# Kernel tuning notes

Hardware: AMD Instinct MI355X
Metric: run time of the kernel (lower is better)

Reference implementation:

```python
import jax, jax.numpy as jnp
import numpy as np

N_NODES = 100000
N_EDGES = 600000
F_IN = 128
F_OUT = 128


def setup_inputs() -> dict:
    key = jax.random.key(0)
    ks = jax.random.split(key, 9)
    stdv = 1.0 / np.sqrt(F_OUT)
    return {
        "x": jax.random.normal(ks[0], (N_NODES, F_IN), dtype=jnp.float32),
        "weight": jax.random.uniform(ks[1], (F_IN, F_OUT), dtype=jnp.float32, minval=-stdv, maxval=stdv),
        "bias": jax.random.uniform(ks[2], (F_OUT,), dtype=jnp.float32, minval=-stdv, maxval=stdv),
        "vals0": jax.random.uniform(ks[3], (N_EDGES,), dtype=jnp.float32),
        "vals1": jax.random.uniform(ks[4], (N_EDGES,), dtype=jnp.float32),
        "rows0": jax.random.randint(ks[5], (N_EDGES,), 0, N_NODES, dtype=jnp.int32),
        "cols0": jax.random.randint(ks[6], (N_EDGES,), 0, N_NODES, dtype=jnp.int32),
        "rows1": jax.random.randint(ks[7], (N_EDGES,), 0, N_NODES, dtype=jnp.int32),
        "cols1": jax.random.randint(ks[8], (N_EDGES,), 0, N_NODES, dtype=jnp.int32),
    }


def _spmm(rows, cols, vals, dense, n):
    # COO sparse [n,n] @ dense [n,f]: gather source rows, scale, scatter-add to dest rows
    msgs = dense[cols] * vals[:, None]          # [E, f]
    return jax.ops.segment_sum(msgs, rows, num_segments=n)


def reference(x, weight, bias, vals0, vals1, rows0, cols0, rows1, cols1):
    n = x.shape[0]
    support = x @ weight                         # [N, F_OUT] dense GEMM
    out = _spmm(rows0, cols0, vals0, support, n) \
        + _spmm(rows1, cols1, vals1, support, n)
    return out + bias
```

## Files before the change

kernel.cpp:

```cpp
#include <hip/hip_runtime.h>


#define FDIM 128
#define EPB 2048

typedef __attribute__((ext_vector_type(8))) short short8;
typedef __attribute__((ext_vector_type(4))) float floatx4;

__device__ __forceinline__ unsigned short f32_to_bf16(float f) {
    unsigned int u = __float_as_uint(f);
    unsigned int r = u + 0x7fffu + ((u >> 16) & 1u);
    return (unsigned short)(r >> 16);
}

__device__ __forceinline__ float bf16_lo(unsigned int u) {
    return __uint_as_float((u & 0xffffu) << 16);
}
__device__ __forceinline__ float bf16_hi(unsigned int u) {
    return __uint_as_float(u & 0xffff0000u);
}

__global__ __launch_bounds__(256) void prep(const float* __restrict__ w,
                                            unsigned short* __restrict__ wt,
                                            int* __restrict__ zero_ptr, int zero_ints) {
    int bid = blockIdx.x;
    if (bid < 64) {
        int idx = bid * 256 + threadIdx.x;
        int nn = idx >> 7, k = idx & 127;
        wt[idx] = f32_to_bf16(w[(size_t)k * FDIM + nn]);
    } else {
        int idx = (bid - 64) * 256 + threadIdx.x;
        if (idx < zero_ints) zero_ptr[idx] = 0;
    }
}

__global__ __launch_bounds__(256) void gemm_hist(const float* __restrict__ x,
                                                 const unsigned short* __restrict__ wt,
                                                 unsigned short* __restrict__ support,
                                                 int n,
                                                 const int* __restrict__ rows0,
                                                 const int* __restrict__ rows1,
                                                 int* __restrict__ count,
                                                 int* __restrict__ rank,
                                                 int E, int GB) {
    if ((int)blockIdx.x >= GB) {
        int gid = (blockIdx.x - GB) * 256 + threadIdx.x;
        if (gid < 2 * E) {
            int r = (gid < E) ? rows0[gid] : rows1[gid - E];
            rank[gid] = atomicAdd(&count[r], 1);
        }
        return;
    }
    const int tid = threadIdx.x;
    const int wv = tid >> 6, lane = tid & 63;
    const int quad = lane >> 4, lr = lane & 15;
    const int rbase = blockIdx.x * 256 + wv * 64;
    if (rbase >= n) return;

    short8 b[8][4];
    #pragma unroll
    for (int nt = 0; nt < 8; ++nt)
        #pragma unroll
        for (int ks = 0; ks < 4; ++ks)
            b[nt][ks] = *(const short8*)(wt + (size_t)(nt * 16 + lr) * FDIM + ks * 32 + quad * 8);

    for (int t = 0; t < 4; ++t) {
        const int row0 = rbase + t * 16;
        if (row0 >= n) break;
        const int arow = row0 + lr;
        const bool rowok = arow < n;
        const float* xr = x + (size_t)arow * FDIM;

        floatx4 acc[8];
        #pragma unroll
        for (int nt = 0; nt < 8; ++nt) acc[nt] = (floatx4)0.f;

        #pragma unroll
        for (int ks = 0; ks < 4; ++ks) {
            float4 lo = rowok ? *(const float4*)(xr + ks * 32 + quad * 8)     : make_float4(0.f,0.f,0.f,0.f);
            float4 hi = rowok ? *(const float4*)(xr + ks * 32 + quad * 8 + 4) : make_float4(0.f,0.f,0.f,0.f);
            short8 a;
            a[0] = (short)f32_to_bf16(lo.x); a[1] = (short)f32_to_bf16(lo.y);
            a[2] = (short)f32_to_bf16(lo.z); a[3] = (short)f32_to_bf16(lo.w);
            a[4] = (short)f32_to_bf16(hi.x); a[5] = (short)f32_to_bf16(hi.y);
            a[6] = (short)f32_to_bf16(hi.z); a[7] = (short)f32_to_bf16(hi.w);
            #pragma unroll
            for (int nt = 0; nt < 8; ++nt)
                acc[nt] = __builtin_amdgcn_mfma_f32_16x16x32_bf16(a, b[nt][ks], acc[nt], 0, 0, 0);
        }

        #pragma unroll
        for (int i = 0; i < 4; ++i) {
            int row = row0 + quad * 4 + i;
            if (row < n) {
                #pragma unroll
                for (int nt = 0; nt < 8; ++nt)
                    support[(size_t)row * FDIM + nt * 16 + lr] = f32_to_bf16(acc[nt][i]);
            }
        }
    }
}

__device__ __forceinline__ int block_incl_scan(int v, int tid, int* lds) {
    int lane = tid & 63, wv = tid >> 6;
    #pragma unroll
    for (int d = 1; d < 64; d <<= 1) {
        int y = __shfl_up(v, d);
        if (lane >= d) v += y;
    }
    if (lane == 63) lds[wv] = v;
    __syncthreads();
    if (wv == 0 && lane < 4) {
        int s = lds[lane];
        #pragma unroll
        for (int d = 1; d < 4; d <<= 1) {
            int y = __shfl_up(s, d);
            if (lane >= d) s += y;
        }
        lds[4 + lane] = s;
    }
    __syncthreads();
    int add = (wv > 0) ? lds[4 + wv - 1] : 0;
    return v + add;
}

__global__ __launch_bounds__(256) void rowptr_scan(const int* __restrict__ count,
                                                   int* __restrict__ rowptr,
                                                   int* __restrict__ gcur, int n) {
    __shared__ int lds[8];
    __shared__ int base;
    int tid = threadIdx.x;
    int idx = blockIdx.x * 256 + tid;
    int v = (idx < n) ? count[idx] : 0;
    int inc = block_incl_scan(v, tid, lds);
    if (tid == 255) base = atomicAdd(gcur, inc);
    __syncthreads();
    if (idx < n) rowptr[idx] = base + inc - v;
}

__global__ __launch_bounds__(256) void scatter_row(
    const int* __restrict__ rows0, const int* __restrict__ cols0, const float* __restrict__ vals0,
    const int* __restrict__ rows1, const int* __restrict__ cols1, const float* __restrict__ vals1,
    const int* __restrict__ rank, const int* __restrict__ rowptr,
    int2* __restrict__ rec, int E, int nper) {
    const int p = blockIdx.x & 7;
    const int base = (blockIdx.x >> 3) * EPB;
    const int tid = threadIdx.x;
    #pragma unroll
    for (int it = 0; it < EPB / 256; ++it) {
        int gid = base + it * 256 + tid;
        if (gid < 2 * E) {
            int r = (gid < E) ? rows0[gid] : rows1[gid - E];
            if (r / nper == p) {
                int c; float v;
                if (gid < E) { c = cols0[gid]; v = vals0[gid]; }
                else         { int e = gid - E; c = cols1[e]; v = vals1[e]; }
                rec[rowptr[r] + rank[gid]] = make_int2(c, __float_as_int(v));
            }
        }
    }
}

__global__ __launch_bounds__(256) void pull_csr(const unsigned short* __restrict__ support,
                                                const int* __restrict__ rowptr,
                                                const int* __restrict__ count,
                                                const int2* __restrict__ rec,
                                                const float* __restrict__ bias,
                                                float* __restrict__ out, int n) {
    int wid = (blockIdx.x * 256 + threadIdx.x) >> 6;
    int lane = threadIdx.x & 63;
    if (wid >= n) return;
    int beg = rowptr[wid];
    int end = beg + count[wid];
    float ax = 0.f, ay = 0.f;
    const char* sp = (const char*)support;
    const unsigned loff = (unsigned)lane << 2;

    for (int base = beg; base < end; base += 64) {
        int m = end - base; if (m > 64) m = 64;
        long long pk = 0;
        if (lane < m) pk = *(const long long*)&rec[base + lane];
        int j = 0;
        for (; j + 8 <= m; j += 8) {
            long long p0 = __shfl(pk, j);
            long long p1 = __shfl(pk, j + 1);
            long long p2 = __shfl(pk, j + 2);
            long long p3 = __shfl(pk, j + 3);
            long long p4 = __shfl(pk, j + 4);
            long long p5 = __shfl(pk, j + 5);
            long long p6 = __shfl(pk, j + 6);
            long long p7 = __shfl(pk, j + 7);
            unsigned u0 = *(const unsigned*)(sp + (((unsigned)p0) << 8) + loff);
            unsigned u1 = *(const unsigned*)(sp + (((unsigned)p1) << 8) + loff);
            unsigned u2 = *(const unsigned*)(sp + (((unsigned)p2) << 8) + loff);
            unsigned u3 = *(const unsigned*)(sp + (((unsigned)p3) << 8) + loff);
            unsigned u4 = *(const unsigned*)(sp + (((unsigned)p4) << 8) + loff);
            unsigned u5 = *(const unsigned*)(sp + (((unsigned)p5) << 8) + loff);
            unsigned u6 = *(const unsigned*)(sp + (((unsigned)p6) << 8) + loff);
            unsigned u7 = *(const unsigned*)(sp + (((unsigned)p7) << 8) + loff);
            float v0 = __int_as_float((int)(p0 >> 32));
            float v1 = __int_as_float((int)(p1 >> 32));
            float v2 = __int_as_float((int)(p2 >> 32));
            float v3 = __int_as_float((int)(p3 >> 32));
            float v4 = __int_as_float((int)(p4 >> 32));
            float v5 = __int_as_float((int)(p5 >> 32));
            float v6 = __int_as_float((int)(p6 >> 32));
            float v7 = __int_as_float((int)(p7 >> 32));
            ax += v0 * bf16_lo(u0); ay += v0 * bf16_hi(u0);
            ax += v1 * bf16_lo(u1); ay += v1 * bf16_hi(u1);
            ax += v2 * bf16_lo(u2); ay += v2 * bf16_hi(u2);
            ax += v3 * bf16_lo(u3); ay += v3 * bf16_hi(u3);
            ax += v4 * bf16_lo(u4); ay += v4 * bf16_hi(u4);
            ax += v5 * bf16_lo(u5); ay += v5 * bf16_hi(u5);
            ax += v6 * bf16_lo(u6); ay += v6 * bf16_hi(u6);
            ax += v7 * bf16_lo(u7); ay += v7 * bf16_hi(u7);
        }
        for (; j + 4 <= m; j += 4) {
            long long p0 = __shfl(pk, j);
            long long p1 = __shfl(pk, j + 1);
            long long p2 = __shfl(pk, j + 2);
            long long p3 = __shfl(pk, j + 3);
            unsigned u0 = *(const unsigned*)(sp + (((unsigned)p0) << 8) + loff);
            unsigned u1 = *(const unsigned*)(sp + (((unsigned)p1) << 8) + loff);
            unsigned u2 = *(const unsigned*)(sp + (((unsigned)p2) << 8) + loff);
            unsigned u3 = *(const unsigned*)(sp + (((unsigned)p3) << 8) + loff);
            float v0 = __int_as_float((int)(p0 >> 32));
            float v1 = __int_as_float((int)(p1 >> 32));
            float v2 = __int_as_float((int)(p2 >> 32));
            float v3 = __int_as_float((int)(p3 >> 32));
            ax += v0 * bf16_lo(u0); ay += v0 * bf16_hi(u0);
            ax += v1 * bf16_lo(u1); ay += v1 * bf16_hi(u1);
            ax += v2 * bf16_lo(u2); ay += v2 * bf16_hi(u2);
            ax += v3 * bf16_lo(u3); ay += v3 * bf16_hi(u3);
        }
        for (; j < m; ++j) {
            long long p = __shfl(pk, j);
            unsigned u = *(const unsigned*)(sp + (((unsigned)p) << 8) + loff);
            float v = __int_as_float((int)(p >> 32));
            ax += v * bf16_lo(u); ay += v * bf16_hi(u);
        }
    }
    float2 b = *(const float2*)(bias + lane * 2);
    *(float2*)(out + (size_t)wid * FDIM + lane * 2) = make_float2(ax + b.x, ay + b.y);
}

__global__ __launch_bounds__(256) void init_bias(const float* __restrict__ bias,
                                                 float* __restrict__ out, int n) {
    int idx = blockIdx.x * 256 + threadIdx.x;
    int total = n * (FDIM / 4);
    if (idx < total) {
        int j = (idx & (FDIM / 4 - 1)) * 4;
        float4 b = *(const float4*)(bias + j);
        *(float4*)(out + (size_t)idx * 4) = b;
    }
}

__global__ __launch_bounds__(256) void scatter_bf16(
    const unsigned short* __restrict__ support,
    const int* __restrict__ rows0, const int* __restrict__ cols0, const float* __restrict__ vals0,
    const int* __restrict__ rows1, const int* __restrict__ cols1, const float* __restrict__ vals1,
    float* __restrict__ out, int E) {
    int gid = blockIdx.x * 256 + threadIdx.x;
    int lane = gid & 63;
    int eg = gid >> 6;
    if (eg >= 2 * E) return;
    int r, c; float v;
    if (eg < E) { r = rows0[eg]; c = cols0[eg]; v = vals0[eg]; }
    else        { int e = eg - E; r = rows1[e]; c = cols1[e]; v = vals1[e]; }
    unsigned int u = *(const unsigned int*)(support + (size_t)c * FDIM + lane * 2);
    float sx = bf16_lo(u);
    float sy = bf16_hi(u);
    float* op = out + (size_t)r * FDIM + lane * 2;
    atomicAdd(op,     sx * v);
    atomicAdd(op + 1, sy * v);
}

static inline size_t align256(size_t v) { return (v + 255) & ~(size_t)255; }

extern "C" void kernel_launch(void* const* d_in, const int* in_sizes, int n_in,
                              void* d_out, int out_size, void* d_ws, size_t ws_size,
                              hipStream_t stream) {
    const float* x     = (const float*)d_in[0];
    const float* w     = (const float*)d_in[1];
    const float* bias  = (const float*)d_in[2];
    const float* vals0 = (const float*)d_in[3];
    const float* vals1 = (const float*)d_in[4];
    const int*   rows0 = (const int*)d_in[5];
    const int*   cols0 = (const int*)d_in[6];
    const int*   rows1 = (const int*)d_in[7];
    const int*   cols1 = (const int*)d_in[8];
    const int n = in_sizes[0] / FDIM;
    const int E = in_sizes[3];
    float* out = (float*)d_out;

    const int NB = (n + 255) / 256;

    size_t off = 0;
    unsigned short* support = (unsigned short*)((char*)d_ws + off);
    off = align256(off + (size_t)n * FDIM * 2);
    unsigned short* wt = (unsigned short*)((char*)d_ws + off);
    off = align256(off + (size_t)FDIM * FDIM * 2);
    size_t count_off = off;
    int*  count  = (int*)((char*)d_ws + off);  off = align256(off + (size_t)n * 4);
    int*  gcur   = (int*)((char*)d_ws + off);  off = align256(off + 4);
    size_t zero_bytes = off - count_off;
    int*  rowptr = (int*)((char*)d_ws + off);  off = align256(off + (size_t)n * 4);
    int*  rank   = (int*)((char*)d_ws + off);  off = align256(off + (size_t)2 * E * 4);
    int2* rec    = (int2*)((char*)d_ws + off); off = align256(off + (size_t)2 * E * 8);

    const bool fits = off <= ws_size;
    const int GB = (n + 255) / 256;
    const int HB = fits ? (2 * E + 255) / 256 : 0;

    int zero_ints = fits ? (int)(zero_bytes / 4) : 0;
    int zb = (zero_ints + 255) / 256;
    prep<<<64 + zb, 256, 0, stream>>>(w, wt, (int*)((char*)d_ws + count_off), zero_ints);

    gemm_hist<<<GB + HB, 256, 0, stream>>>(x, wt, support, n,
                                           rows0, rows1, count, rank, E, GB);

    if (fits) {
        rowptr_scan<<<NB, 256, 0, stream>>>(count, rowptr, gcur, n);
        int nper = (n + 7) / 8;
        int ntiles = (2 * E + EPB - 1) / EPB;
        scatter_row<<<ntiles * 8, 256, 0, stream>>>(rows0, cols0, vals0,
                                                    rows1, cols1, vals1,
                                                    rank, rowptr, rec, E, nper);
        pull_csr<<<(n + 3) / 4, 256, 0, stream>>>(support, rowptr, count, rec, bias, out, n);
    } else {
        int total4 = n * (FDIM / 4);
        init_bias<<<(total4 + 255) / 256, 256, 0, stream>>>(bias, out, n);
        long long tthreads = 2LL * E * 64;
        int blocks = (int)((tthreads + 255) / 256);
        scatter_bf16<<<blocks, 256, 0, stream>>>(support, rows0, cols0, vals0,
                                                 rows1, cols1, vals1, out, E);
    }
}
```

Measured before the change: 264.4 us.

## Split GEMM from histogram, stage weights in LDS, use atomic cursors for CSR scatter

The fused GEMM+histogram kernel is split in two. The GEMM now stages the bf16 weight tile in LDS and processes 64 rows per block, where before each wave held the weights in registers across 64 rows. The histogram no longer stores per-edge ranks. Instead, scatter claims slots with atomics on a per-row cursor that the scan initialises, which removes the rank array's write and read traffic. The cost is one extra kernel launch, loss of overlap between the GEMM and the histogram, and nondeterministic edge order within each row.

```diff
diff --git a/kernel.cpp b/kernel.cpp
--- a/kernel.cpp
+++ b/kernel.cpp
@@ -34,69 +34,72 @@
     }
 }
 
-__global__ __launch_bounds__(256) void gemm_hist(const float* __restrict__ x,
-                                                 const unsigned short* __restrict__ wt,
-                                                 unsigned short* __restrict__ support,
-                                                 int n,
-                                                 const int* __restrict__ rows0,
+__global__ __launch_bounds__(256) void hist_rows(const int* __restrict__ rows0,
                                                  const int* __restrict__ rows1,
-                                                 int* __restrict__ count,
-                                                 int* __restrict__ rank,
-                                                 int E, int GB) {
-    if ((int)blockIdx.x >= GB) {
-        int gid = (blockIdx.x - GB) * 256 + threadIdx.x;
-        if (gid < 2 * E) {
-            int r = (gid < E) ? rows0[gid] : rows1[gid - E];
-            rank[gid] = atomicAdd(&count[r], 1);
-        }
-        return;
-    }
+                                                 int* __restrict__ count, int E) {
+    int gid = blockIdx.x * 256 + threadIdx.x;
+    if (gid >= 2 * E) return;
+    int r = (gid < E) ? rows0[gid] : rows1[gid - E];
+    atomicAdd(&count[r], 1);
+}
+
+__global__ __launch_bounds__(256) void gemm_lds(const float* __restrict__ x,
+                                                const unsigned short* __restrict__ wt,
+                                                unsigned short* __restrict__ support,
+                                                int n) {
+    __shared__ __align__(16) short Bs[128][136];
     const int tid = threadIdx.x;
+
+    #pragma unroll
+    for (int i = 0; i < 8; ++i) {
+        int idx = tid + i * 256;
+        int r = idx >> 4, c8 = idx & 15;
+        *(short8*)&Bs[r][c8 * 8] = *(const short8*)(wt + (size_t)r * FDIM + c8 * 8);
+    }
+    __syncthreads();
+
     const int wv = tid >> 6, lane = tid & 63;
     const int quad = lane >> 4, lr = lane & 15;
-    const int rbase = blockIdx.x * 256 + wv * 64;
-    if (rbase >= n) return;
-
-    short8 b[8][4];
-    #pragma unroll
-    for (int nt = 0; nt < 8; ++nt)
+    const int row0 = blockIdx.x * 64 + wv * 16;
+    if (row0 >= n) return;
+
+    const int arow = row0 + lr;
+    const bool rowok = arow < n;
+    const float* xr = x + (size_t)arow * FDIM;
+
+    float4 f[8];
+    #pragma unroll
+    for (int ks = 0; ks < 4; ++ks) {
+        f[2 * ks]     = rowok ? *(const float4*)(xr + ks * 32 + quad * 8)     : make_float4(0.f,0.f,0.f,0.f);
+        f[2 * ks + 1] = rowok ? *(const float4*)(xr + ks * 32 + quad * 8 + 4) : make_float4(0.f,0.f,0.f,0.f);
+    }
+
+    floatx4 acc[8];
+    #pragma unroll
+    for (int nt = 0; nt < 8; ++nt) acc[nt] = (floatx4)0.f;
+
+    #pragma unroll
+    for (int ks = 0; ks < 4; ++ks) {
+        float4 lo = f[2 * ks], hi = f[2 * ks + 1];
+        short8 a;
+        a[0] = (short)f32_to_bf16(lo.x); a[1] = (short)f32_to_bf16(lo.y);
+        a[2] = (short)f32_to_bf16(lo.z); a[3] = (short)f32_to_bf16(lo.w);
+        a[4] = (short)f32_to_bf16(hi.x); a[5] = (short)f32_to_bf16(hi.y);
+        a[6] = (short)f32_to_bf16(hi.z); a[7] = (short)f32_to_bf16(hi.w);
         #pragma unroll
-        for (int ks = 0; ks < 4; ++ks)
-            b[nt][ks] = *(const short8*)(wt + (size_t)(nt * 16 + lr) * FDIM + ks * 32 + quad * 8);
-
-    for (int t = 0; t < 4; ++t) {
-        const int row0 = rbase + t * 16;
-        if (row0 >= n) break;
-        const int arow = row0 + lr;
-        const bool rowok = arow < n;
-        const float* xr = x + (size_t)arow * FDIM;
-
-        floatx4 acc[8];
-        #pragma unroll
-        for (int nt = 0; nt < 8; ++nt) acc[nt] = (floatx4)0.f;
-
-        #pragma unroll
-        for (int ks = 0; ks < 4; ++ks) {
-            float4 lo = rowok ? *(const float4*)(xr + ks * 32 + quad * 8)     : make_float4(0.f,0.f,0.f,0.f);
-            float4 hi = rowok ? *(const float4*)(xr + ks * 32 + quad * 8 + 4) : make_float4(0.f,0.f,0.f,0.f);
-            short8 a;
-            a[0] = (short)f32_to_bf16(lo.x); a[1] = (short)f32_to_bf16(lo.y);
-            a[2] = (short)f32_to_bf16(lo.z); a[3] = (short)f32_to_bf16(lo.w);
-            a[4] = (short)f32_to_bf16(hi.x); a[5] = (short)f32_to_bf16(hi.y);
-            a[6] = (short)f32_to_bf16(hi.z); a[7] = (short)f32_to_bf16(hi.w);
+        for (int nt = 0; nt < 8; ++nt) {
+            short8 b = *(const short8*)&Bs[nt * 16 + lr][ks * 32 + quad * 8];
+            acc[nt] = __builtin_amdgcn_mfma_f32_16x16x32_bf16(a, b, acc[nt], 0, 0, 0);
+        }
+    }
+
+    #pragma unroll
+    for (int i = 0; i < 4; ++i) {
+        int row = row0 + quad * 4 + i;
+        if (row < n) {
             #pragma unroll
             for (int nt = 0; nt < 8; ++nt)
-                acc[nt] = __builtin_amdgcn_mfma_f32_16x16x32_bf16(a, b[nt][ks], acc[nt], 0, 0, 0);
-        }
-
-        #pragma unroll
-        for (int i = 0; i < 4; ++i) {
-            int row = row0 + quad * 4 + i;
-            if (row < n) {
-                #pragma unroll
-                for (int nt = 0; nt < 8; ++nt)
-                    support[(size_t)row * FDIM + nt * 16 + lr] = f32_to_bf16(acc[nt][i]);
-            }
+                support[(size_t)row * FDIM + nt * 16 + lr] = f32_to_bf16(acc[nt][i]);
         }
     }
 }
@@ -126,6 +129,7 @@
 
 __global__ __launch_bounds__(256) void rowptr_scan(const int* __restrict__ count,
                                                    int* __restrict__ rowptr,
+                                                   int* __restrict__ cursor,
                                                    int* __restrict__ gcur, int n) {
     __shared__ int lds[8];
     __shared__ int base;
@@ -135,15 +139,20 @@
     int inc = block_incl_scan(v, tid, lds);
     if (tid == 255) base = atomicAdd(gcur, inc);
     __syncthreads();
-    if (idx < n) rowptr[idx] = base + inc - v;
-}
-
-__global__ __launch_bounds__(256) void scatter_row(
+    if (idx < n) {
+        int p = base + inc - v;
+        rowptr[idx] = p;
+        cursor[idx] = p;
+    }
+}
+
+__global__ __launch_bounds__(256) void scatter_cur(
     const int* __restrict__ rows0, const int* __restrict__ cols0, const float* __restrict__ vals0,
     const int* __restrict__ rows1, const int* __restrict__ cols1, const float* __restrict__ vals1,
-    const int* __restrict__ rank, const int* __restrict__ rowptr,
+    int* __restrict__ cursor,
     int2* __restrict__ rec, int E, int nper) {
     const int p = blockIdx.x & 7;
+    const int rlo = p * nper;
     const int base = (blockIdx.x >> 3) * EPB;
     const int tid = threadIdx.x;
     #pragma unroll
@@ -151,11 +160,12 @@
         int gid = base + it * 256 + tid;
         if (gid < 2 * E) {
             int r = (gid < E) ? rows0[gid] : rows1[gid - E];
-            if (r / nper == p) {
+            if ((unsigned)(r - rlo) < (unsigned)nper) {
                 int c; float v;
                 if (gid < E) { c = cols0[gid]; v = vals0[gid]; }
                 else         { int e = gid - E; c = cols1[e]; v = vals1[e]; }
-                rec[rowptr[r] + rank[gid]] = make_int2(c, __float_as_int(v));
+                int pos = atomicAdd(&cursor[r], 1);
+                rec[pos] = make_int2(c, __float_as_int(v));
             }
         }
     }
@@ -163,7 +173,7 @@
 
 __global__ __launch_bounds__(256) void pull_csr(const unsigned short* __restrict__ support,
                                                 const int* __restrict__ rowptr,
-                                                const int* __restrict__ count,
+                                                const int* __restrict__ cursor,
                                                 const int2* __restrict__ rec,
                                                 const float* __restrict__ bias,
                                                 float* __restrict__ out, int n) {
@@ -171,7 +181,7 @@
     int lane = threadIdx.x & 63;
     if (wid >= n) return;
     int beg = rowptr[wid];
-    int end = beg + count[wid];
+    int end = cursor[wid];
     float ax = 0.f, ay = 0.f;
     const char* sp = (const char*)support;
     const unsigned loff = (unsigned)lane << 2;
@@ -305,28 +315,27 @@
     int*  gcur   = (int*)((char*)d_ws + off);  off = align256(off + 4);
     size_t zero_bytes = off - count_off;
     int*  rowptr = (int*)((char*)d_ws + off);  off = align256(off + (size_t)n * 4);
-    int*  rank   = (int*)((char*)d_ws + off);  off = align256(off + (size_t)2 * E * 4);
+    int*  cursor = (int*)((char*)d_ws + off);  off = align256(off + (size_t)n * 4);
     int2* rec    = (int2*)((char*)d_ws + off); off = align256(off + (size_t)2 * E * 8);
 
     const bool fits = off <= ws_size;
-    const int GB = (n + 255) / 256;
-    const int HB = fits ? (2 * E + 255) / 256 : 0;
 
     int zero_ints = fits ? (int)(zero_bytes / 4) : 0;
     int zb = (zero_ints + 255) / 256;
     prep<<<64 + zb, 256, 0, stream>>>(w, wt, (int*)((char*)d_ws + count_off), zero_ints);
 
-    gemm_hist<<<GB + HB, 256, 0, stream>>>(x, wt, support, n,
-                                           rows0, rows1, count, rank, E, GB);
+    gemm_lds<<<(n + 63) / 64, 256, 0, stream>>>(x, wt, support, n);
 
     if (fits) {
-        rowptr_scan<<<NB, 256, 0, stream>>>(count, rowptr, gcur, n);
+        int eb = (2 * E + 255) / 256;
+        hist_rows<<<eb, 256, 0, stream>>>(rows0, rows1, count, E);
+        rowptr_scan<<<NB, 256, 0, stream>>>(count, rowptr, cursor, gcur, n);
         int nper = (n + 7) / 8;
         int ntiles = (2 * E + EPB - 1) / EPB;
-        scatter_row<<<ntiles * 8, 256, 0, stream>>>(rows0, cols0, vals0,
+        scatter_cur<<<ntiles * 8, 256, 0, stream>>>(rows0, cols0, vals0,
                                                     rows1, cols1, vals1,
-                                                    rank, rowptr, rec, E, nper);
-        pull_csr<<<(n + 3) / 4, 256, 0, stream>>>(support, rowptr, count, rec, bias, out, n);
+                                                    cursor, rec, E, nper);
+        pull_csr<<<(n + 3) / 4, 256, 0, stream>>>(support, rowptr, cursor, rec, bias, out, n);
     } else {
         int total4 = n * (FDIM / 4);
         init_bias<<<(total4 + 255) / 256, 256, 0, stream>>>(bias, out, n);
```

After: 287.1 us. 8.6% more time.
